# Optimization experiments

Measured on AMD Instinct MI355X. Metric: run time of the kernel, lower is better.

Reference implementation:

```python
import jax, jax.numpy as jnp
import numpy as np

N = 100000      # nodes
E = 1000000     # edges
IN = 512
H = [512, 256]
C = 64          # n_classes
K = 10          # propagation steps
ALPHA = 0.1


def _glorot(key, shape):
    lim = np.sqrt(6.0 / (shape[0] + shape[1])).astype(np.float32)
    return jax.random.uniform(key, shape, jnp.float32, -lim, lim)


def setup_inputs() -> dict:
    key = jax.random.key(0)
    ks = jax.random.split(key, 6)
    features = jax.random.normal(ks[0], (N, IN), jnp.float32)
    edge_index = jax.random.randint(ks[1], (2, E), 0, N)  # int32/64 src,dst
    W0 = _glorot(ks[2], (H[0], IN)); b0 = jnp.zeros((H[0],), jnp.float32)
    W1 = _glorot(ks[3], (H[1], H[0])); b1 = jnp.zeros((H[1],), jnp.float32)
    W2 = _glorot(ks[4], (C, H[1])); b2 = jnp.zeros((C,), jnp.float32)
    return dict(features=features, edge_index=edge_index,
                W0=W0, b0=b0, W1=W1, b1=b1, W2=W2, b2=b2)


def _appnp(h, src, dst):
    # DGL APPNPConv: symmetric normalization D_out^{-1/2} A D_in^{-1/2},
    # degrees clamped to min 1; h_{t+1} = (1-a) * norm_agg + a * h_0.
    ones = jnp.ones(src.shape, h.dtype)
    deg_out = jax.ops.segment_sum(ones, src, num_segments=N)
    deg_in = jax.ops.segment_sum(ones, dst, num_segments=N)
    norm_src = jnp.maximum(deg_out, 1.0) ** -0.5  # [N]
    norm_dst = jnp.maximum(deg_in, 1.0) ** -0.5   # [N]
    h0 = h
    for _ in range(K):
        msg = (h * norm_src[:, None])[src]                     # [E, C] gather
        agg = jax.ops.segment_sum(msg, dst, num_segments=N)    # [N, C] scatter-add
        h = (1.0 - ALPHA) * agg * norm_dst[:, None] + ALPHA * h0
    return h


def reference(features, edge_index, W0, b0, W1, b1, W2, b2):
    src, dst = edge_index[0], edge_index[1]
    h = jax.nn.relu(features @ W0.T + b0)   # [N, 512]
    h = jax.nn.relu(h @ W1.T + b1)          # [N, 256]
    h = h @ W2.T + b2                       # [N, 64] logits
    return _appnp(h, src, dst)
```

## Files before the change

### kernel.cpp

```cpp
#include <hip/hip_runtime.h>
#include <hip/hip_bf16.h>

#define NN_NODES 100000
#define NE_EDGES 1000000
#define D_IN 512
#define D_H0 512
#define D_H1 256
#define D_C  64

using f32x4  = __attribute__((ext_vector_type(4))) float;
using h16x8  = __attribute__((ext_vector_type(8))) _Float16;

static __device__ __forceinline__ void gll16(const _Float16* g, _Float16* l){
    __builtin_amdgcn_global_load_lds(
        (const __attribute__((address_space(1))) unsigned int*)g,
        (__attribute__((address_space(3))) unsigned int*)l, 16, 0, 0);
}

__global__ __launch_bounds__(256) void tof16_tiled_kernel(
    const float* __restrict__ w, _Float16* __restrict__ o, int R, int K)
{
    int i = blockIdx.x * 256 + threadIdx.x;
    int n8 = R * (K >> 3);
    if (i >= n8) return;
    int kd = K >> 3;
    int r  = i / kd;
    int c0 = (i - r * kd) * 8;
    const f32x4 a = *(const f32x4*)(w + (size_t)r * K + c0);
    const f32x4 b = *(const f32x4*)(w + (size_t)r * K + c0 + 4);
    h16x8 h;
    #pragma unroll
    for (int j = 0; j < 4; j++){
        h[j]   = (_Float16)a[j];
        h[j+4] = (_Float16)b[j];
    }
    size_t off = ((size_t)(r >> 7) * (K >> 5) + (c0 >> 5)) * 4096
               + (size_t)(r & 127) * 32 + (c0 & 31);
    *(h16x8*)(o + off) = h;
}

template<bool RELU, int OMODE, int BN_T, int NBN, int KK>
__global__ __launch_bounds__(256, 3) void gemm_kernel(
    const _Float16* __restrict__ A,
    const _Float16* __restrict__ B,
    const float* __restrict__ bias,
    void* __restrict__ O1, _Float16* __restrict__ O2, const float* __restrict__ scale,
    int M, int NNc, int xq, int xr)
{
    constexpr int NTK = KK / 32;
    constexpr int NF  = BN_T / 32;

    __shared__ _Float16 sA[3][128 * 32];

    const int tid  = threadIdx.x;
    const int lane = tid & 63;
    const int wv   = tid >> 6;
    const int wm   = wv >> 1;
    const int wn   = wv & 1;
    const int fr   = lane & 15;
    const int fc   = lane >> 4;

    const int bid = blockIdx.x;
    const int xcd = bid & 7;
    const int i8  = bid >> 3;
    const int L   = ((xcd < xr) ? xcd * (xq + 1) : xr * (xq + 1) + (xcd - xr) * xq) + i8;
    const int mt  = L / NBN;
    const int bn  = L - mt * NBN;
    const int bm0 = mt * 128;
    const int bn0 = bn * BN_T;

    const int loff = (lane >> 2) * 32 + ((lane & 3) ^ ((lane >> 3) & 3)) * 8;

    f32x4 acc[4][NF] = {};
    h16x8 b0f[NF], b1f[NF];

    auto stageA = [&](int b, int t){
        const _Float16* as = A + ((size_t)mt * NTK + t) * 4096;
        gll16(as + (wv * 2)     * 512 + loff, sA[b] + (wv * 2)     * 512);
        gll16(as + (wv * 2 + 1) * 512 + loff, sA[b] + (wv * 2 + 1) * 512);
    };

    auto loadB = [&](h16x8 (&bf)[NF], int t){
        const _Float16* bs = B + ((size_t)bn * NTK + t) * 4096;
        #pragma unroll
        for (int nf = 0; nf < NF; nf++)
            bf[nf] = *(const h16x8*)(bs + (wn * (BN_T / 2) + nf * 16 + fr) * 32 + fc * 8);
    };

    auto compute = [&](h16x8 (&bf)[NF], int b3){
        h16x8 af[4];
        #pragma unroll
        for (int mf = 0; mf < 4; mf++){
            int r = wm * 64 + mf * 16 + fr;
            int c = (fc ^ ((r >> 1) & 3)) * 8;
            af[mf] = *(const h16x8*)&sA[b3][r * 32 + c];
        }
        __builtin_amdgcn_s_setprio(1);
        #pragma unroll
        for (int mf = 0; mf < 4; mf++)
            #pragma unroll
            for (int nf = 0; nf < NF; nf++)
                acc[mf][nf] = __builtin_amdgcn_mfma_f32_16x16x32_f16(af[mf], bf[nf], acc[mf][nf], 0, 0, 0);
        __builtin_amdgcn_s_setprio(0);
    };

    loadB(b0f, 0);
    stageA(0, 0);
    stageA(1, 1);
    #pragma unroll
    for (int t = 0; t < NTK; t++){
        if (t + 1 < NTK){
            if ((t + 1) & 1) loadB(b1f, t + 1);
            else             loadB(b0f, t + 1);
        }
        if (t + 2 < NTK) stageA((t + 2) % 3, t + 2);
        if (t + 2 < NTK){
            if constexpr (NF == 4) asm volatile("s_waitcnt vmcnt(8)" ::: "memory");
            else                   asm volatile("s_waitcnt vmcnt(6)" ::: "memory");
        } else if (t + 1 < NTK){
            if constexpr (NF == 4) asm volatile("s_waitcnt vmcnt(6)" ::: "memory");
            else                   asm volatile("s_waitcnt vmcnt(4)" ::: "memory");
        } else {
            asm volatile("s_waitcnt vmcnt(0)" ::: "memory");
        }
        __builtin_amdgcn_s_barrier();
        asm volatile("" ::: "memory");
        if (t & 1) compute(b1f, t % 3);
        else       compute(b0f, t % 3);
        asm volatile("" ::: "memory");
        __builtin_amdgcn_s_barrier();
        asm volatile("" ::: "memory");
    }

    #pragma unroll
    for (int mf = 0; mf < 4; mf++){
        #pragma unroll
        for (int nf = 0; nf < NF; nf++){
            #pragma unroll
            for (int r = 0; r < 4; r++){
                int rg = bm0 + wm * 64 + mf * 16 + fc * 4 + r;
                int cg = bn0 + wn * (BN_T / 2) + nf * 16 + fr;
                if (rg < M){
                    float v = acc[mf][nf][r] + bias[cg];
                    if constexpr (RELU) v = fmaxf(v, 0.f);
                    if constexpr (OMODE == 1){
                        size_t o = ((size_t)mt * (NNc >> 5) + (cg >> 5)) * 4096
                                 + (size_t)(rg & 127) * 32 + (cg & 31);
                        ((_Float16*)O1)[o] = (_Float16)v;
                    } else {
                        ((_Float16*)O1)[(size_t)rg * NNc + cg] = (_Float16)v;
                        O2[(size_t)rg * NNc + cg] = (_Float16)(v * scale[rg]);
                    }
                }
            }
        }
    }
}

__global__ void degrees_kernel(const int* __restrict__ src, const int* __restrict__ dst,
                               int* __restrict__ dout, int* __restrict__ din){
    int e = blockIdx.x * blockDim.x + threadIdx.x;
    if (e < NE_EDGES){
        atomicAdd(&dout[src[e]], 1);
        atomicAdd(&din[dst[e]], 1);
    }
}

__global__ void norm_kernel(const int* __restrict__ dout, const int* __restrict__ din,
                            float* __restrict__ ns, float* __restrict__ nd, int n){
    int i = blockIdx.x * blockDim.x + threadIdx.x;
    if (i < n){
        ns[i] = rsqrtf((float)(dout[i] > 1 ? dout[i] : 1));
        nd[i] = rsqrtf((float)(din[i]  > 1 ? din[i]  : 1));
    }
}

__global__ __launch_bounds__(256) void scan1_kernel(const int* __restrict__ din,
                                                    int* __restrict__ part,
                                                    int* __restrict__ bsum, int n){
    __shared__ int s[256];
    int i = blockIdx.x * 256 + threadIdx.x;
    int v = (i < n) ? din[i] : 0;
    s[threadIdx.x] = v;
    __syncthreads();
    for (int off = 1; off < 256; off <<= 1){
        int t = (threadIdx.x >= off) ? s[threadIdx.x - off] : 0;
        __syncthreads();
        s[threadIdx.x] += t;
        __syncthreads();
    }
    if (i < n) part[i] = s[threadIdx.x];
    if (threadIdx.x == 255) bsum[blockIdx.x] = s[255];
}

__global__ __launch_bounds__(512) void scan2_kernel(int* __restrict__ bsum, int nb){
    __shared__ int s[512];
    int v = (threadIdx.x < nb) ? bsum[threadIdx.x] : 0;
    s[threadIdx.x] = v;
    __syncthreads();
    for (int off = 1; off < 512; off <<= 1){
        int t = (threadIdx.x >= off) ? s[threadIdx.x - off] : 0;
        __syncthreads();
        s[threadIdx.x] += t;
        __syncthreads();
    }
    if (threadIdx.x < nb) bsum[threadIdx.x] = s[threadIdx.x];
}

__global__ void scan3_kernel(const int* __restrict__ part, const int* __restrict__ din,
                             const int* __restrict__ bsum, int* __restrict__ offs,
                             int* __restrict__ cur, int n){
    int i = blockIdx.x * 256 + threadIdx.x;
    if (i < n){
        int base = (blockIdx.x > 0) ? bsum[blockIdx.x - 1] : 0;
        int excl = base + part[i] - din[i];
        offs[i] = excl;
        cur[i]  = excl;
    }
}

__global__ void fill_kernel(const int* __restrict__ src, const int* __restrict__ dst,
                            int* __restrict__ cur, int* __restrict__ csr){
    int e = blockIdx.x * blockDim.x + threadIdx.x;
    if (e < NE_EDGES){
        int d = dst[e];
        int pos = atomicAdd(&cur[d], 1);
        csr[pos] = src[e];
    }
}

__global__ __launch_bounds__(256) void propagate_kernel(
    const _Float16* __restrict__ hs, const _Float16* __restrict__ h0h,
    float* __restrict__ hout, _Float16* __restrict__ houts,
    const int* __restrict__ offs, const int* __restrict__ din,
    const int* __restrict__ csr,
    const float* __restrict__ ns, const float* __restrict__ nd)
{
    int t    = blockIdx.x * 256 + threadIdx.x;
    int node = t >> 3;
    int gl   = t & 7;
    if (node >= NN_NODES) return;
    int start = offs[node];
    int deg   = din[node];
    float acc[8] = {};
    int j = 0;
    for (; j + 2 <= deg; j += 2){
        int s0 = csr[start + j];
        int s1 = csr[start + j + 1];
        h16x8 v0 = *(const h16x8*)(hs + (size_t)s0 * D_C + gl * 8);
        h16x8 v1 = *(const h16x8*)(hs + (size_t)s1 * D_C + gl * 8);
        #pragma unroll
        for (int i = 0; i < 8; i++) acc[i] += (float)v0[i] + (float)v1[i];
    }
    if (j < deg){
        int s0 = csr[start + j];
        h16x8 v0 = *(const h16x8*)(hs + (size_t)s0 * D_C + gl * 8);
        #pragma unroll
        for (int i = 0; i < 8; i++) acc[i] += (float)v0[i];
    }
    float ndv = 0.9f * nd[node];
    h16x8 h0v = *(const h16x8*)(h0h + (size_t)node * D_C + gl * 8);
    float out[8];
    #pragma unroll
    for (int i = 0; i < 8; i++) out[i] = acc[i] * ndv + 0.1f * (float)h0v[i];
    if (houts){
        float nsv = ns[node];
        h16x8 o;
        #pragma unroll
        for (int i = 0; i < 8; i++) o[i] = (_Float16)(out[i] * nsv);
        *(h16x8*)(houts + (size_t)node * D_C + gl * 8) = o;
    }
    if (hout){
        f32x4 oa, ob;
        #pragma unroll
        for (int i = 0; i < 4; i++){ oa[i] = out[i]; ob[i] = out[i + 4]; }
        *(f32x4*)(hout + (size_t)node * D_C + gl * 8)     = oa;
        *(f32x4*)(hout + (size_t)node * D_C + gl * 8 + 4) = ob;
    }
}

extern "C" void kernel_launch(void* const* d_in, const int* in_sizes, int n_in,
                              void* d_out, int out_size, void* d_ws, size_t ws_size,
                              hipStream_t stream)
{
    const float* features = (const float*)d_in[0];
    const int*   edge     = (const int*)d_in[1];
    const float* W0 = (const float*)d_in[2];
    const float* b0 = (const float*)d_in[3];
    const float* W1 = (const float*)d_in[4];
    const float* b1 = (const float*)d_in[5];
    const float* W2 = (const float*)d_in[6];
    const float* b2 = (const float*)d_in[7];
    const int* src = edge;
    const int* dst = edge + NE_EDGES;

    char* p = (char*)d_ws;
    auto alloc = [&](size_t bytes) -> char* {
        char* r = p;
        p += (bytes + 255) & ~(size_t)255;
        return r;
    };

    const int MT = (NN_NODES + 127) / 128;
    const size_t FEAT_T = (size_t)MT * 16 * 4096 * 2;
    const size_t HBUFH  = (size_t)NN_NODES * D_C * 2;

    _Float16* w0f = (_Float16*)alloc((size_t)4 * 16 * 4096 * 2);
    _Float16* w1f = (_Float16*)alloc((size_t)2 * 16 * 4096 * 2);
    _Float16* w2f = (_Float16*)alloc((size_t)1 * 8  * 4096 * 2);
    char* R1 = alloc(FEAT_T);
    char* R2 = alloc(FEAT_T);
    int*   deg_out = (int*)alloc((size_t)NN_NODES * 4);
    int*   deg_in  = (int*)alloc((size_t)NN_NODES * 4);
    float* nsrc    = (float*)alloc((size_t)NN_NODES * 4);
    float* ndst    = (float*)alloc((size_t)NN_NODES * 4);
    int*   part    = (int*)alloc((size_t)NN_NODES * 4);
    int*   bsum    = (int*)alloc(2048);
    int*   offs    = (int*)alloc((size_t)NN_NODES * 4);
    int*   cur     = (int*)alloc((size_t)NN_NODES * 4);
    int*   csr     = (int*)alloc((size_t)NE_EDGES * 4);
    if ((size_t)(p - (char*)d_ws) > ws_size) return;

    _Float16* fhf  = (_Float16*)R1;
    _Float16* act2 = (_Float16*)R1;
    _Float16* act1 = (_Float16*)R2;
    _Float16* h0h  = (_Float16*)R2;
    _Float16* h0s  = (_Float16*)(R2 + HBUFH);
    _Float16* hAs  = (_Float16*)(R2 + 2 * HBUFH);
    _Float16* hBs  = (_Float16*)(R2 + 3 * HBUFH);

    hipMemsetAsync(deg_out, 0, (size_t)NN_NODES * 4, stream);
    hipMemsetAsync(deg_in,  0, (size_t)NN_NODES * 4, stream);
    degrees_kernel<<<(NE_EDGES + 255) / 256, 256, 0, stream>>>(src, dst, deg_out, deg_in);
    norm_kernel<<<(NN_NODES + 255) / 256, 256, 0, stream>>>(deg_out, deg_in, nsrc, ndst, NN_NODES);
    int nb = (NN_NODES + 255) / 256;
    scan1_kernel<<<nb, 256, 0, stream>>>(deg_in, part, bsum, NN_NODES);
    scan2_kernel<<<1, 512, 0, stream>>>(bsum, nb);
    scan3_kernel<<<nb, 256, 0, stream>>>(part, deg_in, bsum, offs, cur, NN_NODES);
    fill_kernel<<<(NE_EDGES + 255) / 256, 256, 0, stream>>>(src, dst, cur, csr);

    tof16_tiled_kernel<<<(NN_NODES * D_IN / 8 + 255) / 256, 256, 0, stream>>>(
        features, fhf, NN_NODES, D_IN);
    tof16_tiled_kernel<<<(D_H0 * D_IN / 8 + 255) / 256, 256, 0, stream>>>(W0, w0f, D_H0, D_IN);
    tof16_tiled_kernel<<<(D_H1 * D_H0 / 8 + 255) / 256, 256, 0, stream>>>(W1, w1f, D_H1, D_H0);
    tof16_tiled_kernel<<<(D_C * D_H1 / 8 + 255) / 256, 256, 0, stream>>>(W2, w2f, D_C, D_H1);

    {
        int nwg = MT * 4;
        gemm_kernel<true, 1, 128, 4, 512><<<nwg, 256, 0, stream>>>(
            fhf, w0f, b0, act1, nullptr, nullptr, NN_NODES, D_H0, nwg / 8, nwg % 8);
    }
    {
        int nwg = MT * 2;
        gemm_kernel<true, 1, 128, 2, 512><<<nwg, 256, 0, stream>>>(
            act1, w1f, b1, act2, nullptr, nullptr, NN_NODES, D_H1, nwg / 8, nwg % 8);
    }
    {
        int nwg = MT;
        gemm_kernel<false, 2, 64, 1, 256><<<nwg, 256, 0, stream>>>(
            act2, w2f, b2, h0h, h0s, nsrc, NN_NODES, D_C, nwg / 8, nwg % 8);
    }

    const _Float16* curs = h0s;
    _Float16* bufss[2] = { hAs, hBs };
    int pb = (NN_NODES * 8 + 255) / 256;
    for (int it = 0; it < 10; it++){
        float*    out  = (it == 9) ? (float*)d_out : nullptr;
        _Float16* outs = (it == 9) ? nullptr       : bufss[it & 1];
        propagate_kernel<<<pb, 256, 0, stream>>>(curs, h0h, out, outs, offs, deg_in, csr, nsrc, ndst);
        curs = outs;
    }
}
```

Before: 666.7 us.

## Stage B tiles through LDS with double buffering and narrower GEMM N-tiles

The GEMM kernel now stages B (weights) into shared memory with the same swizzled global-to-LDS loads as A, replacing per-wave register loads of B. The A buffer goes from three stages to two, and the hand-tuned vmcnt waits are replaced by a simple double-buffered loop with __syncthreads. The first two GEMMs use 64-wide N tiles, which doubles the workgroup count, and the occupancy hint rises to 4. This is meant to cut redundant global B loads and raise occupancy. The costs are an extra barrier per K step, less prefetch depth, and A tiles being re-read across more N blocks.

```diff
diff --git a/kernel.cpp b/kernel.cpp
--- a/kernel.cpp
+++ b/kernel.cpp
@@ -40,17 +40,21 @@
 }
 
 template<bool RELU, int OMODE, int BN_T, int NBN, int KK>
-__global__ __launch_bounds__(256, 3) void gemm_kernel(
+__global__ __launch_bounds__(256, 4) void gemm_kernel(
     const _Float16* __restrict__ A,
     const _Float16* __restrict__ B,
     const float* __restrict__ bias,
     void* __restrict__ O1, _Float16* __restrict__ O2, const float* __restrict__ scale,
     int M, int NNc, int xq, int xr)
 {
-    constexpr int NTK = KK / 32;
-    constexpr int NF  = BN_T / 32;
-
-    __shared__ _Float16 sA[3][128 * 32];
+    constexpr int NTK  = KK / 32;
+    constexpr int NF   = BN_T / 32;
+    constexpr int BBLK = BN_T / 16;
+    constexpr int TOT  = 8 + BBLK;
+    constexpr int LPW  = TOT / 4;
+
+    __shared__ _Float16 sA[2][128 * 32];
+    __shared__ _Float16 sB[2][BN_T * 32];
 
     const int tid  = threadIdx.x;
     const int lane = tid & 63;
@@ -69,31 +73,38 @@
     const int bm0 = mt * 128;
     const int bn0 = bn * BN_T;
 
+    const int bslab = bn0 >> 7;
+    const int binsl = bn0 & 127;
+
     const int loff = (lane >> 2) * 32 + ((lane & 3) ^ ((lane >> 3) & 3)) * 8;
 
     f32x4 acc[4][NF] = {};
-    h16x8 b0f[NF], b1f[NF];
-
-    auto stageA = [&](int b, int t){
+
+    auto stage = [&](int b, int t){
         const _Float16* as = A + ((size_t)mt * NTK + t) * 4096;
-        gll16(as + (wv * 2)     * 512 + loff, sA[b] + (wv * 2)     * 512);
-        gll16(as + (wv * 2 + 1) * 512 + loff, sA[b] + (wv * 2 + 1) * 512);
+        const _Float16* bs = B + ((size_t)bslab * NTK + t) * 4096 + binsl * 32;
+        #pragma unroll
+        for (int u = 0; u < LPW; u++){
+            int idx = u * 4 + wv;
+            if (idx < 8) gll16(as + idx * 512 + loff, sA[b] + idx * 512);
+            else         gll16(bs + (idx - 8) * 512 + loff, sB[b] + (idx - 8) * 512);
+        }
     };
 
-    auto loadB = [&](h16x8 (&bf)[NF], int t){
-        const _Float16* bs = B + ((size_t)bn * NTK + t) * 4096;
-        #pragma unroll
-        for (int nf = 0; nf < NF; nf++)
-            bf[nf] = *(const h16x8*)(bs + (wn * (BN_T / 2) + nf * 16 + fr) * 32 + fc * 8);
-    };
-
-    auto compute = [&](h16x8 (&bf)[NF], int b3){
+    auto compute = [&](int b){
+        h16x8 bf[NF];
+        #pragma unroll
+        for (int nf = 0; nf < NF; nf++){
+            int r = wn * (BN_T / 2) + nf * 16 + fr;
+            int c = (fc ^ ((r >> 1) & 3)) * 8;
+            bf[nf] = *(const h16x8*)&sB[b][r * 32 + c];
+        }
         h16x8 af[4];
         #pragma unroll
         for (int mf = 0; mf < 4; mf++){
             int r = wm * 64 + mf * 16 + fr;
             int c = (fc ^ ((r >> 1) & 3)) * 8;
-            af[mf] = *(const h16x8*)&sA[b3][r * 32 + c];
+            af[mf] = *(const h16x8*)&sA[b][r * 32 + c];
         }
         __builtin_amdgcn_s_setprio(1);
         #pragma unroll
@@ -104,32 +115,14 @@
         __builtin_amdgcn_s_setprio(0);
     };
 
-    loadB(b0f, 0);
-    stageA(0, 0);
-    stageA(1, 1);
-    #pragma unroll
+    stage(0, 0);
+    __syncthreads();
+    int cur = 0;
     for (int t = 0; t < NTK; t++){
-        if (t + 1 < NTK){
-            if ((t + 1) & 1) loadB(b1f, t + 1);
-            else             loadB(b0f, t + 1);
-        }
-        if (t + 2 < NTK) stageA((t + 2) % 3, t + 2);
-        if (t + 2 < NTK){
-            if constexpr (NF == 4) asm volatile("s_waitcnt vmcnt(8)" ::: "memory");
-            else                   asm volatile("s_waitcnt vmcnt(6)" ::: "memory");
-        } else if (t + 1 < NTK){
-            if constexpr (NF == 4) asm volatile("s_waitcnt vmcnt(6)" ::: "memory");
-            else                   asm volatile("s_waitcnt vmcnt(4)" ::: "memory");
-        } else {
-            asm volatile("s_waitcnt vmcnt(0)" ::: "memory");
-        }
-        __builtin_amdgcn_s_barrier();
-        asm volatile("" ::: "memory");
-        if (t & 1) compute(b1f, t % 3);
-        else       compute(b0f, t % 3);
-        asm volatile("" ::: "memory");
-        __builtin_amdgcn_s_barrier();
-        asm volatile("" ::: "memory");
+        if (t + 1 < NTK) stage(cur ^ 1, t + 1);
+        compute(cur);
+        __syncthreads();
+        cur ^= 1;
     }
 
     #pragma unroll
@@ -346,13 +339,13 @@
     tof16_tiled_kernel<<<(D_C * D_H1 / 8 + 255) / 256, 256, 0, stream>>>(W2, w2f, D_C, D_H1);
 
     {
+        int nwg = MT * 8;
+        gemm_kernel<true, 1, 64, 8, 512><<<nwg, 256, 0, stream>>>(
+            fhf, w0f, b0, act1, nullptr, nullptr, NN_NODES, D_H0, nwg / 8, nwg % 8);
+    }
+    {
         int nwg = MT * 4;
-        gemm_kernel<true, 1, 128, 4, 512><<<nwg, 256, 0, stream>>>(
-            fhf, w0f, b0, act1, nullptr, nullptr, NN_NODES, D_H0, nwg / 8, nwg % 8);
-    }
-    {
-        int nwg = MT * 2;
-        gemm_kernel<true, 1, 128, 2, 512><<<nwg, 256, 0, stream>>>(
+        gemm_kernel<true, 1, 64, 4, 512><<<nwg, 256, 0, stream>>>(
             act1, w1f, b1, act2, nullptr, nullptr, NN_NODES, D_H1, nwg / 8, nwg % 8);
     }
     {
```

Result: faster. 635.9 us (-4.6%).
